# Kernel optimization log

Hardware: AMD Instinct MI355X
Metric: run time of the kernel (lower is better)

The kernel has to match this reference:

```python
import jax, jax.numpy as jnp
import numpy as np

E = 8            # num_experts
K = 2            # top-k
CF = 1.25        # capacity_factor
NOISE_STD = 1.0 / E   # noise_mult / num_experts


def setup_inputs() -> dict:
    key = jax.random.key(0)
    ks = jax.random.split(key, 4)
    B, S, D, H = 8, 1024, 768, 3072
    x = jax.random.normal(ks[0], (B, S, D), jnp.float32)
    router_w = jax.random.normal(ks[1], (D, E), jnp.float32) * 0.02
    fc1_w = jax.random.normal(ks[2], (E, D, H), jnp.float32) * 0.02
    fc1_b = jnp.zeros((E, H), jnp.float32)
    fc2_w = jax.random.normal(ks[3], (E, H, D), jnp.float32) * 0.02
    fc2_b = jnp.zeros((E, D), jnp.float32)
    return dict(x=x, router_w=router_w, fc1_w=fc1_w, fc1_b=fc1_b, fc2_w=fc2_w, fc2_b=fc2_b)


def reference(x, router_w, fc1_w, fc1_b, fc2_w, fc2_b):
    B, S, D = x.shape
    N = B * S
    A = N * K                                   # total (token, slot) assignments
    capacity = int(round(K * N * CF / E))
    x_flat = x.reshape(N, D)

    # ---- router (eval mode: no noise, no dropout) ----
    logits = (x_flat @ router_w).astype(jnp.float32)          # [N,E]
    clean_probs = jax.nn.softmax(logits, axis=-1)
    noisy_logits = logits
    noisy_probs = jax.nn.softmax(noisy_logits, axis=-1)
    topk_probs, topk_idx = jax.lax.top_k(noisy_probs, K)      # [N,K]
    topk_probs = topk_probs.astype(x.dtype)

    flat_e = topk_idx.reshape(-1)                             # [A]
    expert_counts = jax.ops.segment_sum(jnp.ones((A,), jnp.float32), flat_e, num_segments=E)

    # ---- aux losses ----
    importance = clean_probs.sum(0)
    mi = importance.mean()
    loss_importance = jnp.var(importance) / (mi * mi + 1e-6)
    # kthvalue(noisy_logits, E-K+1) == (E-K+1)-th smallest == sorted[:, E-K]
    threshold = jnp.sort(noisy_logits, axis=-1)[:, E - K][:, None]
    prob_selected = 1.0 - jax.scipy.stats.norm.cdf(threshold - logits, loc=0.0, scale=NOISE_STD)
    load = prob_selected.sum(0)
    ml = load.mean()
    loss_load = jnp.var(load) / (ml * ml + 1e-6)
    aux_loss = 0.5 * (loss_importance + loss_load)

    # ---- priority-based capacity dropping (vectorized over all assignments) ----
    priority = clean_probs.max(-1)                            # [N]
    tok = jnp.repeat(jnp.arange(N, dtype=jnp.int32), K)       # [A] token of each assignment
    kslot = jnp.tile(jnp.arange(K, dtype=jnp.int32), N)       # [A] which top-k slot
    score = priority[tok] - kslot.astype(jnp.float32)         # combined_scores = -k_idx + priority
    # group by expert (ascending), within expert sort by score descending
    sort_key = flat_e.astype(jnp.float32) * (K + 2) - score
    order = jnp.argsort(sort_key)
    e_sorted = flat_e[order]
    counts = jax.ops.segment_sum(jnp.ones((A,), jnp.int32), flat_e, num_segments=E)
    starts = jnp.cumsum(counts) - counts
    rank_sorted = jnp.arange(A, dtype=jnp.int32) - starts[e_sorted]   # position within expert group
    rank = jnp.zeros((A,), jnp.int32).at[order].set(rank_sorted)
    keep = rank < capacity
    dropped = jnp.sum(~keep).astype(jnp.int32)

    # ---- dispatch into fixed [E, capacity] buffer (overflow slot sliced off) ----
    pos = jnp.where(keep, flat_e * capacity + rank, E * capacity)
    dispatch_tok = jnp.zeros((E * capacity + 1,), jnp.int32).at[pos].set(tok)[:-1]
    w_flat = topk_probs.reshape(-1)
    weight_buf = jnp.zeros((E * capacity + 1,), x.dtype).at[pos].set(jnp.where(keep, w_flat, 0.0))[:-1]

    xe = x_flat[dispatch_tok].reshape(E, capacity, D)         # gather
    h = jax.nn.gelu(jnp.einsum('ecd,edh->ech', xe, fc1_w) + fc1_b[:, None, :], approximate=False)
    ye = jnp.einsum('ech,ehd->ecd', h, fc2_w) + fc2_b[:, None, :]
    weighted = ye * weight_buf.reshape(E, capacity, 1)
    # padded slots have weight 0 and token 0 -> contribute nothing
    out_flat = jnp.zeros((N, D), x.dtype).at[dispatch_tok].add(weighted.reshape(E * capacity, D))

    return out_flat.reshape(B, S, D), aux_loss, dropped, expert_counts
```

## Files before the change

kernel.cpp:

```cpp
#include <hip/hip_runtime.h>
#include <hip/hip_bf16.h>
#include <math.h>

#define NTOK 8192
#define DIM  768
#define HDIM 3072
#define NE   8
#define CAP  2560
#define AMAX 16384

typedef __bf16 bf16x8  __attribute__((ext_vector_type(8)));
typedef __bf16 bf16x2  __attribute__((ext_vector_type(2)));
typedef float  floatx4 __attribute__((ext_vector_type(4)));

typedef unsigned int u32_g __attribute__((address_space(1)));
typedef unsigned int u32_l __attribute__((address_space(3)));

__device__ __forceinline__ void gl_lds16(const void* g, void* l) {
  __builtin_amdgcn_global_load_lds((const u32_g*)g, (u32_l*)l, 16, 0, 0);
}

__device__ __forceinline__ float gelu_exact(float v) {
  float z = fabsf(v) * 0.7071067811865475f;
  float t = __builtin_amdgcn_rcpf(1.0f + 0.3275911f * z);
  float p = ((((1.061405429f * t - 1.453152027f) * t + 1.421413741f) * t
              - 0.284496736f) * t + 0.254829592f) * t;
  float e = 1.0f - p * __expf(-z * z);
  e = copysignf(e, v);
  return 0.5f * v * (1.0f + e);
}

__global__ __launch_bounds__(256) void transpose_conv2(
    const float* __restrict__ w1, const float* __restrict__ w2,
    __bf16* __restrict__ o1, __bf16* __restrict__ o2)
{
  const int which = blockIdx.z;
  const float* src = which ? w2 : w1;
  __bf16* dst = which ? o2 : o1;
  const int Kd = which ? HDIM : DIM;
  const int Nd = which ? DIM : HDIM;
  const int e = blockIdx.y;
  const int tilesK = Kd >> 6;
  const int bk = blockIdx.x % tilesK, bn = blockIdx.x / tilesK;
  __shared__ float T[64][65];
  const float* se = src + (size_t)e * Kd * Nd;
  const int k0 = bk * 64, n0 = bn * 64;
  const int tid = threadIdx.x;
#pragma unroll
  for (int it = 0; it < 16; ++it) {
    int flat = tid + it * 256;
    int kk = flat >> 6, nn = flat & 63;
    T[kk][nn] = se[(size_t)(k0 + kk) * Nd + n0 + nn];
  }
  __syncthreads();
  const int n = tid >> 2, kg = tid & 3;
  bf16x8 v0, v1;
#pragma unroll
  for (int q = 0; q < 8; ++q) v0[q] = (__bf16)T[kg * 16 + q][n];
#pragma unroll
  for (int q = 0; q < 8; ++q) v1[q] = (__bf16)T[kg * 16 + 8 + q][n];
  __bf16* de = dst + (size_t)e * Nd * Kd + (size_t)(n0 + n) * Kd + k0 + kg * 16;
  *(bf16x8*)(de) = v0;
  *(bf16x8*)(de + 8) = v1;
}

__global__ __launch_bounds__(256) void router_kernel(
    const float* __restrict__ x, const float* __restrict__ rw,
    int* __restrict__ list_len, double* __restrict__ imp, double* __restrict__ loadacc,
    int* __restrict__ aidx, float* __restrict__ keyarr, float* __restrict__ warr)
{
  __shared__ float Wl[NE * DIM];
  __shared__ int   lcount[NE], lbase[NE];
  __shared__ int   s_e[32][2], s_pos[32][2];
  __shared__ float s_key[32][2], s_w[32][2];
  const int tid = threadIdx.x;
  for (int i = tid; i < NE * DIM; i += 256) {
    int e = i / DIM, d = i - e * DIM;
    Wl[i] = rw[d * NE + e];
  }
  if (tid < NE) lcount[tid] = 0;
  __syncthreads();
  const int wave = tid >> 6, lane = tid & 63;
  double my_imp = 0.0, my_load = 0.0;

  for (int it = 0; it < 8; ++it) {
    const int t = wave * 8 + it;
    const int n = blockIdx.x * 32 + t;
    const float* xr = x + (size_t)n * DIM;
    float part[NE];
#pragma unroll
    for (int e = 0; e < NE; ++e) part[e] = 0.f;
#pragma unroll
    for (int c = 0; c < DIM / 64; ++c) {
      float xv = xr[c * 64 + lane];
#pragma unroll
      for (int e = 0; e < NE; ++e) part[e] += xv * Wl[e * DIM + c * 64 + lane];
    }
#pragma unroll
    for (int off = 32; off > 0; off >>= 1) {
#pragma unroll
      for (int e = 0; e < NE; ++e) part[e] += __shfl_xor(part[e], off);
    }
    int e0 = 0; float v0 = part[0];
#pragma unroll
    for (int e = 1; e < NE; ++e) if (part[e] > v0) { v0 = part[e]; e0 = e; }
    int e1 = -1; float v1 = -3.4e38f;
#pragma unroll
    for (int e = 0; e < NE; ++e) if (e != e0 && part[e] > v1) { v1 = part[e]; e1 = e; }

    float pexp[NE]; float s = 0.f;
#pragma unroll
    for (int e = 0; e < NE; ++e) { pexp[e] = expf(part[e] - v0); s += pexp[e]; }
    const float inv = 1.0f / s;
    const float pr = inv;
    float w1v = 0.f;
#pragma unroll
    for (int e = 0; e < NE; ++e) if (e == e1) w1v = pexp[e] * inv;

    float myl = 0.f, mypexp = 0.f;
#pragma unroll
    for (int e = 0; e < NE; ++e) if (lane == e) { myl = part[e]; mypexp = pexp[e]; }
    if (lane < NE) {
      my_imp  += (double)(mypexp * inv);
      my_load += (double)(0.5f * erfcf((v1 - myl) * 5.656854249492380f));
    }
    if (lane == 0) {
      int p0 = atomicAdd(&lcount[e0], 1);
      int p1 = atomicAdd(&lcount[e1], 1);
      s_e[t][0] = e0; s_pos[t][0] = p0;
      s_key[t][0] = (float)(e0 * 4) - pr;
      s_w[t][0] = pr;
      s_e[t][1] = e1; s_pos[t][1] = p1;
      s_key[t][1] = (float)(e1 * 4) - (pr - 1.0f);
      s_w[t][1] = w1v;
    }
  }
  __syncthreads();
  if (tid < NE) lbase[tid] = atomicAdd(&list_len[tid], lcount[tid]);
  __syncthreads();
  if (tid < 64) {
    const int t = tid >> 1, sl = tid & 1;
    const int e = s_e[t][sl];
    const int gp = lbase[e] + s_pos[t][sl];
    const int n = blockIdx.x * 32 + t;
    aidx[e * AMAX + gp]   = n * 2 + sl;
    keyarr[e * AMAX + gp] = s_key[t][sl];
    warr[e * AMAX + gp]   = s_w[t][sl];
  }
  if (lane < NE) {
    unsafeAtomicAdd(&imp[lane], my_imp);
    unsafeAtomicAdd(&loadacc[lane], my_load);
  }
}

__global__ __launch_bounds__(256) void compact_kernel(
    const int* __restrict__ list_len, const int* __restrict__ aidx,
    const float* __restrict__ keyarr, const float* __restrict__ warr,
    int* __restrict__ dtok, float* __restrict__ dw,
    const double* __restrict__ imp, const double* __restrict__ loadacc,
    float* __restrict__ out_scalars)
{
  __shared__ float sk[6144];
  __shared__ int   sa[6144];
  const int e = blockIdx.x, tid = threadIdx.x;
  const int C = list_len[e];
  if (C <= CAP) {
    for (int t = tid; t < C; t += 256) {
      int a = aidx[e * AMAX + t];
      dtok[e * CAP + t] = a >> 1;
      dw[e * CAP + t]   = warr[e * AMAX + t];
    }
  } else {
    const bool useL = (C <= 6144);
    if (useL) {
      for (int t = tid; t < C; t += 256) { sk[t] = keyarr[e*AMAX+t]; sa[t] = aidx[e*AMAX+t]; }
      __syncthreads();
    }
    for (int t = tid; t < C; t += 256) {
      float kt = keyarr[e*AMAX+t]; int at = aidx[e*AMAX+t];
      int r = 0;
      for (int u = 0; u < C; ++u) {
        float ku = useL ? sk[u] : keyarr[e*AMAX+u];
        int   au = useL ? sa[u] : aidx[e*AMAX+u];
        if (ku < kt || (ku == kt && au < at)) ++r;
      }
      if (r < CAP) { dtok[e*CAP + r] = at >> 1; dw[e*CAP + r] = warr[e*AMAX+t]; }
    }
  }
  if (e == 0 && tid == 0) {
    double mi = 0, ml = 0;
    for (int i = 0; i < NE; ++i) { mi += imp[i]; ml += loadacc[i]; }
    mi /= NE; ml /= NE;
    double vi = 0, vl = 0;
    for (int i = 0; i < NE; ++i) {
      double di = imp[i] - mi;     vi += di * di;
      double dl = loadacc[i] - ml; vl += dl * dl;
    }
    vi /= NE; vl /= NE;
    double li = vi / (mi * mi + 1e-6), ll = vl / (ml * ml + 1e-6);
    out_scalars[0] = (float)(0.5 * (li + ll));
    int drop = 0;
    for (int i = 0; i < NE; ++i) { int c2 = list_len[i]; if (c2 > CAP) drop += c2 - CAP; }
    out_scalars[1] = (float)drop;
    for (int i = 0; i < NE; ++i) out_scalars[2 + i] = (float)list_len[i];
  }
}

__global__ __launch_bounds__(256) void gather_kernel(
    const float* __restrict__ x, const int* __restrict__ dtok,
    const int* __restrict__ list_len, __bf16* __restrict__ Ag)
{
  const int row  = blockIdx.x * 4 + (threadIdx.x >> 6);
  const int lane = threadIdx.x & 63;
  const int e = row / CAP, slot = row - e * CAP;
  const int kept = min(list_len[e], CAP);
  __bf16* dst = Ag + (size_t)row * DIM;
  if (slot < kept) {
    const float* srcr = x + (size_t)dtok[e * CAP + slot] * DIM;
#pragma unroll
    for (int c = 0; c < DIM / 128; ++c) {
      float2 v = *(const float2*)(srcr + c * 128 + lane * 2);
      bf16x2 o; o[0] = (__bf16)v.x; o[1] = (__bf16)v.y;
      *(bf16x2*)(dst + c * 128 + lane * 2) = o;
    }
  } else {
    bf16x2 z; z[0] = (__bf16)0.f; z[1] = (__bf16)0.f;
#pragma unroll
    for (int c = 0; c < DIM / 128; ++c) *(bf16x2*)(dst + c * 128 + lane * 2) = z;
  }
}

#define BAR() do { asm volatile("" ::: "memory"); __builtin_amdgcn_s_barrier(); asm volatile("" ::: "memory"); } while (0)

#define ST_A(t, bf) do { \
    gl_lds16(gA0 + (size_t)(t) * 32, &S[bf][(wave * 2 + 0) * 512]); \
    gl_lds16(gA1 + (size_t)(t) * 32, &S[bf][(wave * 2 + 1) * 512]); \
  } while (0)

#define ST_B(t, bf) do { \
    gl_lds16(gB0 + (size_t)(t) * 32, &S[bf][8192 + (wave * 2 + 0) * 512]); \
    gl_lds16(gB1 + (size_t)(t) * 32, &S[bf][8192 + (wave * 2 + 1) * 512]); \
  } while (0)

#define RD_A(half, bf) do { \
    _Pragma("unroll") \
    for (int _m = 0; _m < 4; ++_m) \
      aR[_m] = *(const bf16x8*)&S[bf][(wm * 8 + (half) * 4 + _m) * 512 + lane * 8]; \
  } while (0)

#define RD_B(bf) do { \
    _Pragma("unroll") \
    for (int _n = 0; _n < 4; ++_n) \
      bR[_n] = *(const bf16x8*)&S[bf][8192 + (wn * 4 + _n) * 512 + lane * 8]; \
  } while (0)

#define MM(qm) do { \
    __builtin_amdgcn_s_setprio(1); \
    _Pragma("unroll") \
    for (int _m = 0; _m < 4; ++_m) \
      _Pragma("unroll") \
      for (int _n = 0; _n < 4; ++_n) \
        acc[(qm) * 4 + _m][_n] = __builtin_amdgcn_mfma_f32_16x16x32_bf16( \
            aR[_m], bR[_n], acc[(qm) * 4 + _m][_n], 0, 0, 0); \
    __builtin_amdgcn_s_setprio(0); \
  } while (0)

template<int MODE>
__global__ __launch_bounds__(512, 2) void moe_gemm8(
    const __bf16* __restrict__ Aall, const __bf16* __restrict__ BTall,
    const float* __restrict__ bias, __bf16* __restrict__ Hout,
    float* __restrict__ Out, const int* __restrict__ dtok, const float* __restrict__ dww,
    const int* __restrict__ list_len)
{
  const int Kd = MODE ? HDIM : DIM;
  const int Nd = MODE ? DIM : HDIM;
  const int nT = Kd / 32;

  const int i_blk = blockIdx.x;
  const int e = i_blk & 7;
  const int q = i_blk >> 3;
  const int tm = q % 10, tn = q / 10;

  const int kept = min(list_len[e], CAP);
  if (tm >= ((kept + 255) >> 8)) return;

  __shared__ __align__(16) __bf16 S[4][16384];

  const int tid = threadIdx.x, lane = tid & 63, wave = tid >> 6;
  const int wm = wave & 1, wn = wave >> 1;
  const int m0 = tm * 256, n0 = tn * 256;
  const int lr = lane & 15, kq = lane >> 4;

  const __bf16* Abase = Aall + (size_t)e * CAP * Kd;
  const __bf16* Bbase = BTall + (size_t)e * Nd * Kd;

  const __bf16* gA0 = Abase + (size_t)(m0 + (wave * 2 + 0) * 16 + lr) * Kd + kq * 8;
  const __bf16* gA1 = Abase + (size_t)(m0 + (wave * 2 + 1) * 16 + lr) * Kd + kq * 8;
  const __bf16* gB0 = Bbase + (size_t)(n0 + (wave * 2 + 0) * 16 + lr) * Kd + kq * 8;
  const __bf16* gB1 = Bbase + (size_t)(n0 + (wave * 2 + 1) * 16 + lr) * Kd + kq * 8;

  floatx4 acc[8][4];
#pragma unroll
  for (int i = 0; i < 8; ++i)
#pragma unroll
    for (int j = 0; j < 4; ++j) acc[i][j] = (floatx4)0.f;

  bf16x8 aR[4], bR[4];

  ST_A(0, 0); ST_B(0, 0);
  ST_A(1, 1); ST_B(1, 1);
  ST_A(2, 2); ST_B(2, 2);
  __builtin_amdgcn_s_waitcnt(0x0F78);
  BAR();

#pragma unroll 1
  for (int t = 0; t <= nT - 4; ++t) {
    const int bt = t & 3, bs = (t + 3) & 3;
    RD_A(0, bt); RD_B(bt);
    ST_A(t + 3, bs);
    BAR(); MM(0); BAR();
    RD_A(1, bt);
    ST_B(t + 3, bs);
    __builtin_amdgcn_s_waitcnt(0x0F78);
    BAR(); MM(1); BAR();
  }

  {
    int bt = (nT - 3) & 3;
    RD_A(0, bt); RD_B(bt); BAR(); MM(0); BAR();
    RD_A(1, bt);
    __builtin_amdgcn_s_waitcnt(0x0F74);
    BAR(); MM(1); BAR();

    bt = (nT - 2) & 3;
    RD_A(0, bt); RD_B(bt); BAR(); MM(0); BAR();
    RD_A(1, bt);
    __builtin_amdgcn_s_waitcnt(0x0F70);
    BAR(); MM(1); BAR();

    bt = (nT - 1) & 3;
    RD_A(0, bt); RD_B(bt); MM(0);
    RD_A(1, bt); MM(1);
  }

  const int quad = lane >> 4, lcol = lane & 15;
  float bcol[4];
#pragma unroll
  for (int n = 0; n < 4; ++n)
    bcol[n] = bias[e * Nd + n0 + wn * 64 + n * 16 + lcol];

  if (MODE == 0) {
#pragma unroll
    for (int m = 0; m < 8; ++m) {
#pragma unroll
      for (int r = 0; r < 4; ++r) {
        const int row = m0 + wm * 128 + m * 16 + quad * 4 + r;
        __bf16* hrow = Hout + ((size_t)(e * CAP + row)) * Nd + n0 + wn * 64;
#pragma unroll
        for (int n = 0; n < 4; ++n)
          hrow[n * 16 + lcol] = (__bf16)gelu_exact(acc[m][n][r] + bcol[n]);
      }
    }
  } else {
#pragma unroll
    for (int m = 0; m < 8; ++m) {
#pragma unroll
      for (int r = 0; r < 4; ++r) {
        const int row = m0 + wm * 128 + m * 16 + quad * 4 + r;
        const float w = dww[e * CAP + row];
        if (w != 0.0f) {
          const int tok = dtok[e * CAP + row];
          float* orow = Out + (size_t)tok * DIM + n0 + wn * 64;
#pragma unroll
          for (int n = 0; n < 4; ++n)
            unsafeAtomicAdd(&orow[n * 16 + lcol], w * (acc[m][n][r] + bcol[n]));
        }
      }
    }
  }
}

#undef BAR
#undef ST_A
#undef ST_B
#undef RD_A
#undef RD_B
#undef MM

extern "C" void kernel_launch(void* const* d_in, const int* in_sizes, int n_in,
                              void* d_out, int out_size, void* d_ws, size_t ws_size,
                              hipStream_t stream) {
  (void)in_sizes; (void)n_in; (void)out_size; (void)ws_size;
  const float* x  = (const float*)d_in[0];
  const float* rw = (const float*)d_in[1];
  const float* w1 = (const float*)d_in[2];
  const float* b1 = (const float*)d_in[3];
  const float* w2 = (const float*)d_in[4];
  const float* b2 = (const float*)d_in[5];
  float* out = (float*)d_out;
  char* ws = (char*)d_ws;

  int*    list_len = (int*)(ws + 0);
  double* imp      = (double*)(ws + 64);
  double* loadacc  = (double*)(ws + 128);
  int*    dtok     = (int*)(ws + 256);
  float*  dw       = (float*)(ws + 256 + 81920);
  int*    aidx     = (int*)(ws + 164096);
  float*  keyarr   = (float*)(ws + 164096 + 524288);
  float*  warr     = (float*)(ws + 164096 + 1048576);
  __bf16* W1T      = (__bf16*)(ws + 2097152);
  __bf16* W2T      = (__bf16*)(ws + 2097152 + 37748736);
  __bf16* Ag       = (__bf16*)(ws + 2097152 + 2 * 37748736);
  __bf16* hbuf     = (__bf16*)(ws + 2097152 + 2 * 37748736 + 31457280);

  hipMemsetAsync(d_out, 0, (size_t)NTOK * DIM * sizeof(float), stream);
  hipMemsetAsync(ws, 0, 164096, stream);

  transpose_conv2<<<dim3(576, 8, 2), 256, 0, stream>>>(w1, w2, W1T, W2T);
  router_kernel<<<NTOK / 32, 256, 0, stream>>>(x, rw, list_len, imp, loadacc, aidx, keyarr, warr);
  compact_kernel<<<NE, 256, 0, stream>>>(list_len, aidx, keyarr, warr, dtok, dw, imp, loadacc,
                                         out + (size_t)NTOK * DIM);
  gather_kernel<<<(NE * CAP) / 4, 256, 0, stream>>>(x, dtok, list_len, Ag);
  moe_gemm8<0><<<NE * 10 * (HDIM / 256), 512, 0, stream>>>(
      Ag, W1T, b1, hbuf, nullptr, nullptr, nullptr, list_len);
  moe_gemm8<1><<<NE * 10 * (DIM / 256), 512, 0, stream>>>(
      hbuf, W2T, b2, nullptr, out, dtok, dw, list_len);
}
```

Baseline: 533.4 us.

## Make MoE GEMMs persistent over tiles and widen transpose/gather loads

Both expert GEMMs now launch a fixed grid of 256 blocks that loop over each expert's tile list with a stride, skipping unused M tiles inside the loop. Empty tail blocks no longer exit one by one, and the work is spread more evenly across CUs. The transpose and gather kernels switch to float4 loads and wider bf16 stores. The BAR macro drops its compiler memory fences and the main loop is unrolled by 4. Removing the fences risks reordering LDS accesses, and the persistent loop can leave load imbalance when experts have different token counts.

```diff
diff --git a/kernel.cpp b/kernel.cpp
--- a/kernel.cpp
+++ b/kernel.cpp
@@ -10,6 +10,7 @@
 #define AMAX 16384
 
 typedef __bf16 bf16x8  __attribute__((ext_vector_type(8)));
+typedef __bf16 bf16x4  __attribute__((ext_vector_type(4)));
 typedef __bf16 bf16x2  __attribute__((ext_vector_type(2)));
 typedef float  floatx4 __attribute__((ext_vector_type(4)));
 
@@ -47,10 +48,12 @@
   const int k0 = bk * 64, n0 = bn * 64;
   const int tid = threadIdx.x;
 #pragma unroll
-  for (int it = 0; it < 16; ++it) {
-    int flat = tid + it * 256;
-    int kk = flat >> 6, nn = flat & 63;
-    T[kk][nn] = se[(size_t)(k0 + kk) * Nd + n0 + nn];
+  for (int it = 0; it < 4; ++it) {
+    int flat4 = tid + it * 256;
+    int kk = flat4 >> 4, c4 = flat4 & 15;
+    float4 v = *(const float4*)(se + (size_t)(k0 + kk) * Nd + n0 + c4 * 4);
+    T[kk][c4 * 4 + 0] = v.x; T[kk][c4 * 4 + 1] = v.y;
+    T[kk][c4 * 4 + 2] = v.z; T[kk][c4 * 4 + 3] = v.w;
   }
   __syncthreads();
   const int n = tid >> 2, kg = tid & 3;
@@ -218,19 +221,19 @@
   if (slot < kept) {
     const float* srcr = x + (size_t)dtok[e * CAP + slot] * DIM;
 #pragma unroll
-    for (int c = 0; c < DIM / 128; ++c) {
-      float2 v = *(const float2*)(srcr + c * 128 + lane * 2);
-      bf16x2 o; o[0] = (__bf16)v.x; o[1] = (__bf16)v.y;
-      *(bf16x2*)(dst + c * 128 + lane * 2) = o;
+    for (int c = 0; c < DIM / 256; ++c) {
+      float4 v = *(const float4*)(srcr + c * 256 + lane * 4);
+      bf16x4 o; o[0] = (__bf16)v.x; o[1] = (__bf16)v.y; o[2] = (__bf16)v.z; o[3] = (__bf16)v.w;
+      *(bf16x4*)(dst + c * 256 + lane * 4) = o;
     }
   } else {
-    bf16x2 z; z[0] = (__bf16)0.f; z[1] = (__bf16)0.f;
-#pragma unroll
-    for (int c = 0; c < DIM / 128; ++c) *(bf16x2*)(dst + c * 128 + lane * 2) = z;
-  }
-}
-
-#define BAR() do { asm volatile("" ::: "memory"); __builtin_amdgcn_s_barrier(); asm volatile("" ::: "memory"); } while (0)
+    bf16x4 z; z[0] = (__bf16)0.f; z[1] = (__bf16)0.f; z[2] = (__bf16)0.f; z[3] = (__bf16)0.f;
+#pragma unroll
+    for (int c = 0; c < DIM / 256; ++c) *(bf16x4*)(dst + c * 256 + lane * 4) = z;
+  }
+}
+
+#define BAR() __builtin_amdgcn_s_barrier()
 
 #define ST_A(t, bf) do { \
     gl_lds16(gA0 + (size_t)(t) * 32, &S[bf][(wave * 2 + 0) * 512]); \
@@ -275,105 +278,112 @@
   const int Kd = MODE ? HDIM : DIM;
   const int Nd = MODE ? DIM : HDIM;
   const int nT = Kd / 32;
-
-  const int i_blk = blockIdx.x;
-  const int e = i_blk & 7;
-  const int q = i_blk >> 3;
-  const int tm = q % 10, tn = q / 10;
+  const int QN = MODE ? 3 : 12;
+  const int QTOT = 10 * QN;
+
+  const int e = blockIdx.x & 7;
+  const int slot = blockIdx.x >> 3;
 
   const int kept = min(list_len[e], CAP);
-  if (tm >= ((kept + 255) >> 8)) return;
+  const int mUsed = (kept + 255) >> 8;
 
   __shared__ __align__(16) __bf16 S[4][16384];
 
   const int tid = threadIdx.x, lane = tid & 63, wave = tid >> 6;
   const int wm = wave & 1, wn = wave >> 1;
-  const int m0 = tm * 256, n0 = tn * 256;
   const int lr = lane & 15, kq = lane >> 4;
+  const int quad = lane >> 4, lcol = lane & 15;
 
   const __bf16* Abase = Aall + (size_t)e * CAP * Kd;
   const __bf16* Bbase = BTall + (size_t)e * Nd * Kd;
 
-  const __bf16* gA0 = Abase + (size_t)(m0 + (wave * 2 + 0) * 16 + lr) * Kd + kq * 8;
-  const __bf16* gA1 = Abase + (size_t)(m0 + (wave * 2 + 1) * 16 + lr) * Kd + kq * 8;
-  const __bf16* gB0 = Bbase + (size_t)(n0 + (wave * 2 + 0) * 16 + lr) * Kd + kq * 8;
-  const __bf16* gB1 = Bbase + (size_t)(n0 + (wave * 2 + 1) * 16 + lr) * Kd + kq * 8;
-
   floatx4 acc[8][4];
-#pragma unroll
-  for (int i = 0; i < 8; ++i)
-#pragma unroll
-    for (int j = 0; j < 4; ++j) acc[i][j] = (floatx4)0.f;
-
   bf16x8 aR[4], bR[4];
 
-  ST_A(0, 0); ST_B(0, 0);
-  ST_A(1, 1); ST_B(1, 1);
-  ST_A(2, 2); ST_B(2, 2);
-  __builtin_amdgcn_s_waitcnt(0x0F78);
-  BAR();
-
-#pragma unroll 1
-  for (int t = 0; t <= nT - 4; ++t) {
-    const int bt = t & 3, bs = (t + 3) & 3;
-    RD_A(0, bt); RD_B(bt);
-    ST_A(t + 3, bs);
-    BAR(); MM(0); BAR();
-    RD_A(1, bt);
-    ST_B(t + 3, bs);
+  for (int qi = slot; qi < QTOT; qi += 32) {
+    const int tm = qi / QN, tn = qi % QN;
+    if (tm >= mUsed) continue;
+    const int m0 = tm * 256, n0 = tn * 256;
+
+    const __bf16* gA0 = Abase + (size_t)(m0 + (wave * 2 + 0) * 16 + lr) * Kd + kq * 8;
+    const __bf16* gA1 = Abase + (size_t)(m0 + (wave * 2 + 1) * 16 + lr) * Kd + kq * 8;
+    const __bf16* gB0 = Bbase + (size_t)(n0 + (wave * 2 + 0) * 16 + lr) * Kd + kq * 8;
+    const __bf16* gB1 = Bbase + (size_t)(n0 + (wave * 2 + 1) * 16 + lr) * Kd + kq * 8;
+
+#pragma unroll
+    for (int i = 0; i < 8; ++i)
+#pragma unroll
+      for (int j = 0; j < 4; ++j) acc[i][j] = (floatx4)0.f;
+
+    BAR();
+
+    ST_A(0, 0); ST_B(0, 0);
+    ST_A(1, 1); ST_B(1, 1);
+    ST_A(2, 2); ST_B(2, 2);
     __builtin_amdgcn_s_waitcnt(0x0F78);
-    BAR(); MM(1); BAR();
-  }
-
-  {
-    int bt = (nT - 3) & 3;
-    RD_A(0, bt); RD_B(bt); BAR(); MM(0); BAR();
-    RD_A(1, bt);
-    __builtin_amdgcn_s_waitcnt(0x0F74);
-    BAR(); MM(1); BAR();
-
-    bt = (nT - 2) & 3;
-    RD_A(0, bt); RD_B(bt); BAR(); MM(0); BAR();
-    RD_A(1, bt);
-    __builtin_amdgcn_s_waitcnt(0x0F70);
-    BAR(); MM(1); BAR();
-
-    bt = (nT - 1) & 3;
-    RD_A(0, bt); RD_B(bt); MM(0);
-    RD_A(1, bt); MM(1);
-  }
-
-  const int quad = lane >> 4, lcol = lane & 15;
-  float bcol[4];
-#pragma unroll
-  for (int n = 0; n < 4; ++n)
-    bcol[n] = bias[e * Nd + n0 + wn * 64 + n * 16 + lcol];
-
-  if (MODE == 0) {
-#pragma unroll
-    for (int m = 0; m < 8; ++m) {
-#pragma unroll
-      for (int r = 0; r < 4; ++r) {
-        const int row = m0 + wm * 128 + m * 16 + quad * 4 + r;
-        __bf16* hrow = Hout + ((size_t)(e * CAP + row)) * Nd + n0 + wn * 64;
-#pragma unroll
-        for (int n = 0; n < 4; ++n)
-          hrow[n * 16 + lcol] = (__bf16)gelu_exact(acc[m][n][r] + bcol[n]);
+    BAR();
+
+#pragma unroll 4
+    for (int t = 0; t <= nT - 4; ++t) {
+      const int bt = t & 3, bs = (t + 3) & 3;
+      RD_A(0, bt); RD_B(bt);
+      ST_A(t + 3, bs);
+      BAR(); MM(0); BAR();
+      RD_A(1, bt);
+      ST_B(t + 3, bs);
+      __builtin_amdgcn_s_waitcnt(0x0F78);
+      BAR(); MM(1); BAR();
+    }
+
+    {
+      int bt = (nT - 3) & 3;
+      RD_A(0, bt); RD_B(bt); BAR(); MM(0); BAR();
+      RD_A(1, bt);
+      __builtin_amdgcn_s_waitcnt(0x0F74);
+      BAR(); MM(1); BAR();
+
+      bt = (nT - 2) & 3;
+      RD_A(0, bt); RD_B(bt); BAR(); MM(0); BAR();
+      RD_A(1, bt);
+      __builtin_amdgcn_s_waitcnt(0x0F70);
+      BAR(); MM(1); BAR();
+
+      bt = (nT - 1) & 3;
+      RD_A(0, bt); RD_B(bt); MM(0);
+      RD_A(1, bt); MM(1);
+    }
+
+    float bcol[4];
+#pragma unroll
+    for (int n = 0; n < 4; ++n)
+      bcol[n] = bias[e * Nd + n0 + wn * 64 + n * 16 + lcol];
+
+    if (MODE == 0) {
+#pragma unroll
+      for (int m = 0; m < 8; ++m) {
+#pragma unroll
+        for (int r = 0; r < 4; ++r) {
+          const int row = m0 + wm * 128 + m * 16 + quad * 4 + r;
+          __bf16* hrow = Hout + ((size_t)(e * CAP + row)) * Nd + n0 + wn * 64;
+#pragma unroll
+          for (int n = 0; n < 4; ++n)
+            hrow[n * 16 + lcol] = (__bf16)gelu_exact(acc[m][n][r] + bcol[n]);
+        }
       }
-    }
-  } else {
-#pragma unroll
-    for (int m = 0; m < 8; ++m) {
-#pragma unroll
-      for (int r = 0; r < 4; ++r) {
-        const int row = m0 + wm * 128 + m * 16 + quad * 4 + r;
-        const float w = dww[e * CAP + row];
-        if (w != 0.0f) {
-          const int tok = dtok[e * CAP + row];
-          float* orow = Out + (size_t)tok * DIM + n0 + wn * 64;
-#pragma unroll
-          for (int n = 0; n < 4; ++n)
-            unsafeAtomicAdd(&orow[n * 16 + lcol], w * (acc[m][n][r] + bcol[n]));
+    } else {
+#pragma unroll
+      for (int m = 0; m < 8; ++m) {
+#pragma unroll
+        for (int r = 0; r < 4; ++r) {
+          const int row = m0 + wm * 128 + m * 16 + quad * 4 + r;
+          const float w = dww[e * CAP + row];
+          if (w != 0.0f) {
+            const int tok = dtok[e * CAP + row];
+            float* orow = Out + (size_t)tok * DIM + n0 + wn * 64;
+#pragma unroll
+            for (int n = 0; n < 4; ++n)
+              unsafeAtomicAdd(&orow[n * 16 + lcol], w * (acc[m][n][r] + bcol[n]));
+          }
         }
       }
     }
@@ -421,8 +431,6 @@
   compact_kernel<<<NE, 256, 0, stream>>>(list_len, aidx, keyarr, warr, dtok, dw, imp, loadacc,
                                          out + (size_t)NTOK * DIM);
   gather_kernel<<<(NE * CAP) / 4, 256, 0, stream>>>(x, dtok, list_len, Ag);
-  moe_gemm8<0><<<NE * 10 * (HDIM / 256), 512, 0, stream>>>(
-      Ag, W1T, b1, hbuf, nullptr, nullptr, nullptr, list_len);
-  moe_gemm8<1><<<NE * 10 * (DIM / 256), 512, 0, stream>>>(
-      hbuf, W2T, b2, nullptr, out, dtok, dw, list_len);
-}
+  moe_gemm8<0><<<256, 512, 0, stream>>>(Ag, W1T, b1, hbuf, nullptr, nullptr, nullptr, list_len);
+  moe_gemm8<1><<<256, 512, 0, stream>>>(hbuf, W2T, b2, nullptr, out, dtok, dw, list_len);
+}
```

Measured after the change: 544.2 us. +2.0%, slower.

## Replace 4-stage 256x256 MoE GEMM with single-buffered 128x128 tile kernel

Applied to the files above, without the earlier changes.

Swaps the 512-thread, 4-deep-pipelined 256x256-tile expert GEMM for a 256-thread 128x128-tile kernel with one LDS buffer, plain __syncthreads, and no priority hints. Launch bounds change to (256,3), and the grid is re-derived from CAP/128. The transpose kernel now loads rows as float4 instead of scalars. The GEMM change gives up software pipelining and per-block data reuse in exchange for more, smaller blocks, which risks exposed load latency and extra global traffic.

```diff
diff --git a/kernel.cpp b/kernel.cpp
--- a/kernel.cpp
+++ b/kernel.cpp
@@ -47,10 +47,12 @@
   const int k0 = bk * 64, n0 = bn * 64;
   const int tid = threadIdx.x;
 #pragma unroll
-  for (int it = 0; it < 16; ++it) {
-    int flat = tid + it * 256;
-    int kk = flat >> 6, nn = flat & 63;
-    T[kk][nn] = se[(size_t)(k0 + kk) * Nd + n0 + nn];
+  for (int it = 0; it < 4; ++it) {
+    int flat4 = tid + it * 256;
+    int kk = flat4 >> 4, c4 = flat4 & 15;
+    float4 v = *(const float4*)(se + (size_t)(k0 + kk) * Nd + n0 + c4 * 4);
+    T[kk][c4 * 4 + 0] = v.x; T[kk][c4 * 4 + 1] = v.y;
+    T[kk][c4 * 4 + 2] = v.z; T[kk][c4 * 4 + 3] = v.w;
   }
   __syncthreads();
   const int n = tid >> 2, kg = tid & 3;
@@ -230,43 +232,8 @@
   }
 }
 
-#define BAR() do { asm volatile("" ::: "memory"); __builtin_amdgcn_s_barrier(); asm volatile("" ::: "memory"); } while (0)
-
-#define ST_A(t, bf) do { \
-    gl_lds16(gA0 + (size_t)(t) * 32, &S[bf][(wave * 2 + 0) * 512]); \
-    gl_lds16(gA1 + (size_t)(t) * 32, &S[bf][(wave * 2 + 1) * 512]); \
-  } while (0)
-
-#define ST_B(t, bf) do { \
-    gl_lds16(gB0 + (size_t)(t) * 32, &S[bf][8192 + (wave * 2 + 0) * 512]); \
-    gl_lds16(gB1 + (size_t)(t) * 32, &S[bf][8192 + (wave * 2 + 1) * 512]); \
-  } while (0)
-
-#define RD_A(half, bf) do { \
-    _Pragma("unroll") \
-    for (int _m = 0; _m < 4; ++_m) \
-      aR[_m] = *(const bf16x8*)&S[bf][(wm * 8 + (half) * 4 + _m) * 512 + lane * 8]; \
-  } while (0)
-
-#define RD_B(bf) do { \
-    _Pragma("unroll") \
-    for (int _n = 0; _n < 4; ++_n) \
-      bR[_n] = *(const bf16x8*)&S[bf][8192 + (wn * 4 + _n) * 512 + lane * 8]; \
-  } while (0)
-
-#define MM(qm) do { \
-    __builtin_amdgcn_s_setprio(1); \
-    _Pragma("unroll") \
-    for (int _m = 0; _m < 4; ++_m) \
-      _Pragma("unroll") \
-      for (int _n = 0; _n < 4; ++_n) \
-        acc[(qm) * 4 + _m][_n] = __builtin_amdgcn_mfma_f32_16x16x32_bf16( \
-            aR[_m], bR[_n], acc[(qm) * 4 + _m][_n], 0, 0, 0); \
-    __builtin_amdgcn_s_setprio(0); \
-  } while (0)
-
 template<int MODE>
-__global__ __launch_bounds__(512, 2) void moe_gemm8(
+__global__ __launch_bounds__(256, 3) void moe_gemm97(
     const __bf16* __restrict__ Aall, const __bf16* __restrict__ BTall,
     const float* __restrict__ bias, __bf16* __restrict__ Hout,
     float* __restrict__ Out, const int* __restrict__ dtok, const float* __restrict__ dww,
@@ -275,72 +242,56 @@
   const int Kd = MODE ? HDIM : DIM;
   const int Nd = MODE ? DIM : HDIM;
   const int nT = Kd / 32;
-
-  const int i_blk = blockIdx.x;
-  const int e = i_blk & 7;
-  const int q = i_blk >> 3;
-  const int tm = q % 10, tn = q / 10;
+  const int TM = CAP / 128;
+
+  const int e = blockIdx.x & 7;
+  const int q = blockIdx.x >> 3;
+  const int tm = q % TM, tn = q / TM;
 
   const int kept = min(list_len[e], CAP);
-  if (tm >= ((kept + 255) >> 8)) return;
-
-  __shared__ __align__(16) __bf16 S[4][16384];
+  if (tm >= ((kept + 127) >> 7)) return;
+
+  __shared__ __align__(16) __bf16 S[8192];
 
   const int tid = threadIdx.x, lane = tid & 63, wave = tid >> 6;
   const int wm = wave & 1, wn = wave >> 1;
-  const int m0 = tm * 256, n0 = tn * 256;
+  const int m0 = tm * 128, n0 = tn * 128;
   const int lr = lane & 15, kq = lane >> 4;
 
   const __bf16* Abase = Aall + (size_t)e * CAP * Kd;
   const __bf16* Bbase = BTall + (size_t)e * Nd * Kd;
-
   const __bf16* gA0 = Abase + (size_t)(m0 + (wave * 2 + 0) * 16 + lr) * Kd + kq * 8;
   const __bf16* gA1 = Abase + (size_t)(m0 + (wave * 2 + 1) * 16 + lr) * Kd + kq * 8;
   const __bf16* gB0 = Bbase + (size_t)(n0 + (wave * 2 + 0) * 16 + lr) * Kd + kq * 8;
   const __bf16* gB1 = Bbase + (size_t)(n0 + (wave * 2 + 1) * 16 + lr) * Kd + kq * 8;
 
-  floatx4 acc[8][4];
-#pragma unroll
-  for (int i = 0; i < 8; ++i)
+  floatx4 acc[4][4];
+#pragma unroll
+  for (int i = 0; i < 4; ++i)
 #pragma unroll
     for (int j = 0; j < 4; ++j) acc[i][j] = (floatx4)0.f;
 
   bf16x8 aR[4], bR[4];
 
-  ST_A(0, 0); ST_B(0, 0);
-  ST_A(1, 1); ST_B(1, 1);
-  ST_A(2, 2); ST_B(2, 2);
-  __builtin_amdgcn_s_waitcnt(0x0F78);
-  BAR();
-
 #pragma unroll 1
-  for (int t = 0; t <= nT - 4; ++t) {
-    const int bt = t & 3, bs = (t + 3) & 3;
-    RD_A(0, bt); RD_B(bt);
-    ST_A(t + 3, bs);
-    BAR(); MM(0); BAR();
-    RD_A(1, bt);
-    ST_B(t + 3, bs);
-    __builtin_amdgcn_s_waitcnt(0x0F78);
-    BAR(); MM(1); BAR();
-  }
-
-  {
-    int bt = (nT - 3) & 3;
-    RD_A(0, bt); RD_B(bt); BAR(); MM(0); BAR();
-    RD_A(1, bt);
-    __builtin_amdgcn_s_waitcnt(0x0F74);
-    BAR(); MM(1); BAR();
-
-    bt = (nT - 2) & 3;
-    RD_A(0, bt); RD_B(bt); BAR(); MM(0); BAR();
-    RD_A(1, bt);
-    __builtin_amdgcn_s_waitcnt(0x0F70);
-    BAR(); MM(1); BAR();
-
-    bt = (nT - 1) & 3;
-    RD_A(0, bt); RD_B(bt); MM(0);
-    RD_A(1, bt); MM(1);
+  for (int t = 0; t < nT; ++t) {
+    __syncthreads();
+    gl_lds16(gA0 + t * 32, &S[(wave * 2 + 0) * 512]);
+    gl_lds16(gA1 + t * 32, &S[(wave * 2 + 1) * 512]);
+    gl_lds16(gB0 + t * 32, &S[4096 + (wave * 2 + 0) * 512]);
+    gl_lds16(gB1 + t * 32, &S[4096 + (wave * 2 + 1) * 512]);
+    __syncthreads();
+#pragma unroll
+    for (int m = 0; m < 4; ++m)
+      aR[m] = *(const bf16x8*)&S[(wm * 4 + m) * 512 + lane * 8];
+#pragma unroll
+    for (int n = 0; n < 4; ++n)
+      bR[n] = *(const bf16x8*)&S[4096 + (wn * 4 + n) * 512 + lane * 8];
+#pragma unroll
+    for (int m = 0; m < 4; ++m)
+#pragma unroll
+      for (int n = 0; n < 4; ++n)
+        acc[m][n] = __builtin_amdgcn_mfma_f32_16x16x32_bf16(aR[m], bR[n], acc[m][n], 0, 0, 0);
   }
 
   const int quad = lane >> 4, lcol = lane & 15;
@@ -351,10 +302,10 @@
 
   if (MODE == 0) {
 #pragma unroll
-    for (int m = 0; m < 8; ++m) {
+    for (int m = 0; m < 4; ++m) {
 #pragma unroll
       for (int r = 0; r < 4; ++r) {
-        const int row = m0 + wm * 128 + m * 16 + quad * 4 + r;
+        const int row = m0 + wm * 64 + m * 16 + quad * 4 + r;
         __bf16* hrow = Hout + ((size_t)(e * CAP + row)) * Nd + n0 + wn * 64;
 #pragma unroll
         for (int n = 0; n < 4; ++n)
@@ -363,10 +314,10 @@
     }
   } else {
 #pragma unroll
-    for (int m = 0; m < 8; ++m) {
+    for (int m = 0; m < 4; ++m) {
 #pragma unroll
       for (int r = 0; r < 4; ++r) {
-        const int row = m0 + wm * 128 + m * 16 + quad * 4 + r;
+        const int row = m0 + wm * 64 + m * 16 + quad * 4 + r;
         const float w = dww[e * CAP + row];
         if (w != 0.0f) {
           const int tok = dtok[e * CAP + row];
@@ -379,13 +330,6 @@
     }
   }
 }
-
-#undef BAR
-#undef ST_A
-#undef ST_B
-#undef RD_A
-#undef RD_B
-#undef MM
 
 extern "C" void kernel_launch(void* const* d_in, const int* in_sizes, int n_in,
                               void* d_out, int out_size, void* d_ws, size_t ws_size,
@@ -421,8 +365,8 @@
   compact_kernel<<<NE, 256, 0, stream>>>(list_len, aidx, keyarr, warr, dtok, dw, imp, loadacc,
                                          out + (size_t)NTOK * DIM);
   gather_kernel<<<(NE * CAP) / 4, 256, 0, stream>>>(x, dtok, list_len, Ag);
-  moe_gemm8<0><<<NE * 10 * (HDIM / 256), 512, 0, stream>>>(
+  moe_gemm97<0><<<NE * (CAP / 128) * (HDIM / 128), 256, 0, stream>>>(
       Ag, W1T, b1, hbuf, nullptr, nullptr, nullptr, list_len);
-  moe_gemm8<1><<<NE * 10 * (DIM / 256), 512, 0, stream>>>(
+  moe_gemm97<1><<<NE * (CAP / 128) * (DIM / 128), 256, 0, stream>>>(
       hbuf, W2T, b2, nullptr, out, dtok, dw, list_len);
 }
```

Result: slower. 653.4 us (+22.5%).
